# Optimization experiments

Hardware: AMD Instinct MI355X
Metric: run time of the kernel (lower is better)

Reference implementation:

```python
import jax, jax.numpy as jnp
import numpy as np

N_NODES = 100000
NEG_SLOPE = 0.2  # DGL GATConv default negative_slope


def gat_layer(x, src, dst, W, attn_l, attn_r, bias, n_nodes):
    """Single-head DGL GATConv. x: [N, in], returns [N, out]."""
    h = x @ W                              # [N, out]  fc (no bias)
    el = h @ attn_l                        # [N]
    er = h @ attn_r                        # [N]
    e = el[src] + er[dst]                  # [E]
    e = jnp.where(e >= 0, e, NEG_SLOPE * e)  # leaky_relu
    # segment softmax over incoming edges of each dst node
    m = jax.ops.segment_max(e, dst, num_segments=n_nodes)   # [N]
    ex = jnp.exp(e - m[dst])                                 # [E]
    s = jax.ops.segment_sum(ex, dst, num_segments=n_nodes)  # [N]
    a = ex / s[dst]                                          # [E]
    # weighted aggregate of source features
    msg = a[:, None] * h[src]                                # [E, out]
    out = jax.ops.segment_sum(msg, dst, num_segments=n_nodes)
    return out + bias


def setup_inputs() -> dict:
    key = jax.random.key(0)
    ks = jax.random.split(key, 12)
    n, e = N_NODES, 1600000
    in_f, hid_f, out_f = 128, 64, 64
    inp = {
        "features": jax.random.normal(ks[0], (n, in_f), dtype=jnp.float32),
        "edge_weights": jax.random.uniform(ks[1], (e,), dtype=jnp.float32),
        "src": jax.random.randint(ks[2], (e,), 0, n, dtype=jnp.int32),
        "dst": jax.random.randint(ks[3], (e,), 0, n, dtype=jnp.int32),
        "W1": jax.random.normal(ks[4], (in_f, hid_f), dtype=jnp.float32) * (1.0 / np.sqrt(in_f)),
        "attn_l1": jax.random.normal(ks[5], (hid_f,), dtype=jnp.float32) * 0.1,
        "attn_r1": jax.random.normal(ks[6], (hid_f,), dtype=jnp.float32) * 0.1,
        "bias1": jnp.zeros((hid_f,), dtype=jnp.float32),
        "W2": jax.random.normal(ks[7], (hid_f, out_f), dtype=jnp.float32) * (1.0 / np.sqrt(hid_f)),
        "attn_l2": jax.random.normal(ks[8], (out_f,), dtype=jnp.float32) * 0.1,
        "attn_r2": jax.random.normal(ks[9], (out_f,), dtype=jnp.float32) * 0.1,
        "bias2": jnp.zeros((out_f,), dtype=jnp.float32),
    }
    return inp


def reference(features, edge_weights, src, dst, W1, attn_l1, attn_r1, bias1,
              W2, attn_l2, attn_r2, bias2):
    n = features.shape[0]
    # conv1 -> DGL returns [N, 1, hid]; relu; conv2 -> [N, 1, 1, out]
    h = gat_layer(features, src, dst, W1, attn_l1, attn_r1, bias1, n)  # [N, hid]
    h = jax.nn.relu(h)
    out = gat_layer(h, src, dst, W2, attn_l2, attn_r2, bias2, n)       # [N, out]
    # edge_weights is accepted but unused, matching the original forward
    return out.reshape(n, 1, 1, -1)
```

## Files before the change

### kernel.cpp

```cpp
#include <hip/hip_runtime.h>
#include <hip/hip_fp16.h>

#define NEG_SLOPE 0.2f
#define BKT_SHIFT 9
#define BKT_SIZE (1 << BKT_SHIFT)
#define P1_EPT 16

typedef __attribute__((ext_vector_type(8))) short short8;
typedef __attribute__((ext_vector_type(4))) float float4v;

__device__ inline float readlane_f(float v, int l) {
    return __int_as_float(__builtin_amdgcn_readlane(__float_as_int(v), l));
}
__device__ inline int readlane_i(int v, int l) {
    return __builtin_amdgcn_readlane(v, l);
}
__device__ inline int rfl_i(int v) { return __builtin_amdgcn_readfirstlane(v); }

__device__ inline unsigned short f2bf(float f) {
    unsigned u = __float_as_uint(f);
    unsigned r = u + 0x7FFFu + ((u >> 16) & 1u);
    return (unsigned short)(r >> 16);
}
__device__ inline float bf2f(unsigned short b) {
    return __uint_as_float(((unsigned)b) << 16);
}


__global__ __launch_bounds__(256) void bucket_hist(const int* __restrict__ dst, int e,
                                                   int* __restrict__ bkt_cnt, int nbkt) {
    __shared__ int lc[256];
    int t = threadIdx.x;
    lc[t] = 0;
    __syncthreads();
    int stride = gridDim.x * blockDim.x;
    for (int i = blockIdx.x * blockDim.x + t; i < e; i += stride)
        atomicAdd(&lc[dst[i] >> BKT_SHIFT], 1);
    __syncthreads();
    if (t < nbkt && lc[t]) atomicAdd(&bkt_cnt[t], lc[t]);
}

__global__ void bkt_scan(const int* __restrict__ bkt_cnt, int* __restrict__ bbase,
                         int* __restrict__ gcur, int nbkt, int e_total) {
    __shared__ int tmp[256];
    int t = threadIdx.x;
    int v = (t < nbkt) ? bkt_cnt[t] : 0;
    tmp[t] = v;
    __syncthreads();
    for (int o = 1; o < 256; o <<= 1) {
        int x = tmp[t];
        int y = (t >= o) ? tmp[t - o] : 0;
        __syncthreads();
        tmp[t] = x + y;
        __syncthreads();
    }
    if (t < nbkt) {
        int ex = tmp[t] - v;
        bbase[t] = ex;
        gcur[t] = ex;
    }
    if (t == 0) bbase[nbkt] = e_total;
}

__global__ __launch_bounds__(256) void partition_kernel(
        const int* __restrict__ src, const int* __restrict__ dst, int e,
        int* __restrict__ gcur, int2* __restrict__ part, int nbkt) {
    __shared__ int cnt[4][256];
    __shared__ int base_l[4][256];
    int t = threadIdx.x;
    int wv = t >> 6;
    int cb = blockIdx.x * (256 * P1_EPT);
    for (int i = t; i < 4 * 256; i += 256) ((int*)cnt)[i] = 0;
    __syncthreads();
    int sr[P1_EPT], ds[P1_EPT], rk[P1_EPT];
#pragma unroll
    for (int i = 0; i < P1_EPT; ++i) {
        int eid = cb + t + i * 256;
        if (eid < e) {
            sr[i] = src[eid];
            ds[i] = dst[eid];
            rk[i] = atomicAdd(&cnt[wv][ds[i] >> BKT_SHIFT], 1);
        } else {
            rk[i] = -1;
        }
    }
    __syncthreads();
    if (t < nbkt) {
        int c0 = cnt[0][t], c1 = cnt[1][t], c2 = cnt[2][t], c3 = cnt[3][t];
        int tot = c0 + c1 + c2 + c3;
        int gb = (tot > 0) ? atomicAdd(&gcur[t], tot) : 0;
        base_l[0][t] = gb;
        base_l[1][t] = gb + c0;
        base_l[2][t] = gb + c0 + c1;
        base_l[3][t] = gb + c0 + c1 + c2;
    }
    __syncthreads();
#pragma unroll
    for (int i = 0; i < P1_EPT; ++i) {
        if (rk[i] >= 0) {
            int b = ds[i] >> BKT_SHIFT;
            part[base_l[wv][b] + rk[i]] = make_int2(sr[i], ds[i]);
        }
    }
}

__global__ __launch_bounds__(256) void finesort2(
        const int2* __restrict__ part, const int* __restrict__ bbase,
        int* __restrict__ row_off, int* __restrict__ csr_src, int n, int e_total) {
    __shared__ int cnt[BKT_SIZE];
    __shared__ int cur[BKT_SIZE];
    __shared__ int tmp[256];
    int b = blockIdx.x, t = threadIdx.x;
    int d0 = b << BKT_SHIFT;
    int dlim = min(d0 + BKT_SIZE, n);
    int nloc = dlim - d0;
    for (int i = t; i < BKT_SIZE; i += 256) cnt[i] = 0;
    __syncthreads();
    int base = bbase[b], bend = bbase[b + 1];
    for (int i = base + t; i < bend; i += 256)
        atomicAdd(&cnt[part[i].y - d0], 1);
    __syncthreads();
    int c0 = cnt[2 * t], c1 = cnt[2 * t + 1];
    int s = c0 + c1;
    tmp[t] = s;
    __syncthreads();
    for (int o = 1; o < 256; o <<= 1) {
        int x = tmp[t];
        int y = (t >= o) ? tmp[t - o] : 0;
        __syncthreads();
        tmp[t] = x + y;
        __syncthreads();
    }
    int excl = tmp[t] - s;
    cur[2 * t] = base + excl;
    cur[2 * t + 1] = base + excl + c0;
    __syncthreads();
    for (int i = t; i < nloc; i += 256) row_off[d0 + i] = cur[i];
    if (dlim == n && t == 0) row_off[n] = e_total;
    __syncthreads();
    for (int i = base + t; i < bend; i += 256) {
        int2 p = part[i];
        int pos = atomicAdd(&cur[p.y - d0], 1);
        csr_src[pos] = p.x;
    }
}

__global__ void wprep_kernel(const float* __restrict__ W, unsigned short* __restrict__ wh,
                             unsigned short* __restrict__ wl, int K) {
    int idx = blockIdx.x * blockDim.x + threadIdx.x;
    int KT = K / 32;
    if (idx >= KT * 4 * 64) return;
    int lane = idx & 63;
    int fbkt = idx >> 6;
    int fb = fbkt & 3, kt = fbkt >> 2;
    int q = lane >> 4, c = lane & 15;
    for (int j = 0; j < 8; ++j) {
        float w = W[(kt * 32 + q * 8 + j) * 64 + fb * 16 + c];
        unsigned short hi = f2bf(w);
        wh[idx * 8 + j] = hi;
        wl[idx * 8 + j] = f2bf(w - bf2f(hi));
    }
}

template <int KT>
__global__ __launch_bounds__(256) void gemm_mfma_kernel(
        const float* __restrict__ x, const unsigned short* __restrict__ wh,
        const unsigned short* __restrict__ wl,
        const float* __restrict__ al, const float* __restrict__ ar,
        __half* __restrict__ h16, float* __restrict__ el,
        float* __restrict__ er, int n) {
    constexpr int K = KT * 32;
    constexpr int WFRAG = KT * 4 * 64 * 8;
    __shared__ unsigned short Wh[WFRAG];
    __shared__ unsigned short Wl[WFRAG];
    for (int i = threadIdx.x; i < WFRAG / 8; i += 256) {
        ((float4*)Wh)[i] = ((const float4*)wh)[i];
        ((float4*)Wl)[i] = ((const float4*)wl)[i];
    }
    __syncthreads();

    int lane = threadIdx.x & 63;
    int q = lane >> 4, c = lane & 15;
    int wave = (int)((blockIdx.x * blockDim.x + threadIdx.x) >> 6);
    int nwaves = (gridDim.x * blockDim.x) >> 6;
    int ntiles = (n + 15) >> 4;

    float alv[4], arv[4];
#pragma unroll
    for (int fb = 0; fb < 4; ++fb) {
        alv[fb] = al[fb * 16 + c];
        arv[fb] = ar[fb * 16 + c];
    }

    for (int t = wave; t < ntiles; t += nwaves) {
        int v0 = t * 16;
        int row = min(v0 + c, n - 1);
        const float* xr = x + (size_t)row * K + q * 8;

        short8 Ah[KT], Al[KT];
#pragma unroll
        for (int kt = 0; kt < KT; ++kt) {
            float xv[8];
            *(float4*)&xv[0] = *(const float4*)(xr + kt * 32);
            *(float4*)&xv[4] = *(const float4*)(xr + kt * 32 + 4);
#pragma unroll
            for (int j = 0; j < 8; ++j) {
                unsigned short hi = f2bf(xv[j]);
                Ah[kt][j] = (short)hi;
                Al[kt][j] = (short)f2bf(xv[j] - bf2f(hi));
            }
        }

        float4v acc[4];
#pragma unroll
        for (int fb = 0; fb < 4; ++fb) acc[fb] = (float4v)0.f;

#pragma unroll
        for (int kt = 0; kt < KT; ++kt) {
#pragma unroll
            for (int fb = 0; fb < 4; ++fb) {
                short8 bh = *(const short8*)&Wh[((kt * 4 + fb) * 64 + lane) * 8];
                short8 bl = *(const short8*)&Wl[((kt * 4 + fb) * 64 + lane) * 8];
                acc[fb] = __builtin_amdgcn_mfma_f32_16x16x32_bf16(Ah[kt], bh, acc[fb], 0, 0, 0);
                acc[fb] = __builtin_amdgcn_mfma_f32_16x16x32_bf16(Al[kt], bh, acc[fb], 0, 0, 0);
                acc[fb] = __builtin_amdgcn_mfma_f32_16x16x32_bf16(Ah[kt], bl, acc[fb], 0, 0, 0);
            }
        }

#pragma unroll
        for (int r = 0; r < 4; ++r) {
            int v = v0 + q * 4 + r;
            float pl = 0.f, pr = 0.f;
            bool ok = (v < n);
#pragma unroll
            for (int fb = 0; fb < 4; ++fb) {
                float hv = acc[fb][r];
                if (ok) h16[(size_t)v * 64 + fb * 16 + c] = __float2half(hv);
                pl = fmaf(hv, alv[fb], pl);
                pr = fmaf(hv, arv[fb], pr);
            }
#pragma unroll
            for (int off = 8; off > 0; off >>= 1) {
                pl += __shfl_xor(pl, off);
                pr += __shfl_xor(pr, off);
            }
            if (ok && c == 0) { el[v] = pl; er[v] = pr; }
        }
    }
}

__global__ __launch_bounds__(256) void agg_kernel(
        const int* __restrict__ row_off, const int* __restrict__ csr_src,
        const __half* __restrict__ h16, const float* __restrict__ el,
        const float* __restrict__ er, const float* __restrict__ bias,
        float* __restrict__ out, int n, int do_relu) {
    int lane = threadIdx.x & 63;
    int gwave = rfl_i((int)((blockIdx.x * blockDim.x + threadIdx.x) >> 6));
    int nwaves = (gridDim.x * blockDim.x) >> 6;
    float b = bias[lane];
    for (int v = gwave; v < n; v += nwaves) {
        int rs = rfl_i(row_off[v]), re = rfl_i(row_off[v + 1]);
        float er_v = er[v];
        float acc = 0.f, ssum = 0.f;
        for (int base = rs; base < re; base += 64) {
            int cnt = min(64, re - base);
            int s_e = 0;
            float ex = 0.f;
            if (lane < cnt) {
                s_e = csr_src[base + lane];
                float ev = el[s_e] + er_v;
                ev = (ev >= 0.f) ? ev : NEG_SLOPE * ev;
                ex = __expf(ev);
            }
            float cs = ex;
#pragma unroll
            for (int off = 32; off > 0; off >>= 1) cs += __shfl_xor(cs, off);
            ssum += cs;
            int cnt8 = (cnt + 7) & ~7;
            for (int j = 0; j < cnt8; j += 8) {
                int sj[8];
                float exj[8];
                __half hv[8];
#pragma unroll
                for (int u = 0; u < 8; ++u) {
                    sj[u] = readlane_i(s_e, j + u);
                    exj[u] = readlane_f(ex, j + u);
                    hv[u] = h16[(size_t)sj[u] * 64 + lane];
                }
#pragma unroll
                for (int u = 0; u < 8; ++u)
                    acc = fmaf(exj[u], __half2float(hv[u]), acc);
            }
        }
        float o = (re > rs) ? (acc / ssum + b) : b;
        if (do_relu) o = fmaxf(o, 0.f);
        out[(size_t)v * 64 + lane] = o;
    }
}

extern "C" void kernel_launch(void* const* d_in, const int* in_sizes, int n_in,
                              void* d_out, int out_size, void* d_ws, size_t ws_size,
                              hipStream_t stream) {
    (void)n_in; (void)out_size; (void)ws_size;
    const float* features = (const float*)d_in[0];
    const int*   src = (const int*)d_in[2];
    const int*   dst = (const int*)d_in[3];
    const float* W1  = (const float*)d_in[4];
    const float* al1 = (const float*)d_in[5];
    const float* ar1 = (const float*)d_in[6];
    const float* b1  = (const float*)d_in[7];
    const float* W2  = (const float*)d_in[8];
    const float* al2 = (const float*)d_in[9];
    const float* ar2 = (const float*)d_in[10];
    const float* b2  = (const float*)d_in[11];

    const int n = in_sizes[0] / 128;
    const int e = in_sizes[2];
    float* out = (float*)d_out;

    char* p = (char*)d_ws;
    auto alloc = [&](size_t bytes) -> char* {
        char* q = p;
        p += (bytes + 255) & ~(size_t)255;
        return q;
    };
    int*    row_off = (int*)alloc((size_t)(n + 1) * 4);
    int*    csr_src = (int*)alloc((size_t)e * 4);
    __half* h16     = (__half*)alloc((size_t)n * 64 * 2);
    float*  hr      = (float*)alloc((size_t)n * 64 * 4);
    float*  el      = (float*)alloc((size_t)n * 4);
    float*  er      = (float*)alloc((size_t)n * 4);
    int*    bkt_cnt = (int*)alloc(256 * 4);
    int*    bbase   = (int*)alloc(257 * 4);
    int*    gcur    = (int*)alloc(256 * 4);
    unsigned short* w1h = (unsigned short*)alloc(4 * 4 * 64 * 8 * 2);
    unsigned short* w1l = (unsigned short*)alloc(4 * 4 * 64 * 8 * 2);
    unsigned short* w2h = (unsigned short*)alloc(2 * 4 * 64 * 8 * 2);
    unsigned short* w2l = (unsigned short*)alloc(2 * 4 * 64 * 8 * 2);
    int2*   part    = (int2*)hr;

    const int nbkt = (n + BKT_SIZE - 1) >> BKT_SHIFT;

    wprep_kernel<<<4, 256, 0, stream>>>(W1, w1h, w1l, 128);
    wprep_kernel<<<2, 256, 0, stream>>>(W2, w2h, w2l, 64);

    hipMemsetAsync(bkt_cnt, 0, 256 * 4, stream);
    bucket_hist<<<1024, 256, 0, stream>>>(dst, e, bkt_cnt, nbkt);
    bkt_scan<<<1, 256, 0, stream>>>(bkt_cnt, bbase, gcur, nbkt, e);
    partition_kernel<<<(e + 256 * P1_EPT - 1) / (256 * P1_EPT), 256, 0, stream>>>(
        src, dst, e, gcur, part, nbkt);
    finesort2<<<nbkt, 256, 0, stream>>>(part, bbase, row_off, csr_src, n, e);

    gemm_mfma_kernel<4><<<512, 256, 0, stream>>>(features, w1h, w1l, al1, ar1, h16, el, er, n);
    agg_kernel<<<2048, 256, 0, stream>>>(row_off, csr_src, h16, el, er, b1, hr, n, 1);

    gemm_mfma_kernel<2><<<512, 256, 0, stream>>>(hr, w2h, w2l, al2, ar2, h16, el, er, n);
    agg_kernel<<<2048, 256, 0, stream>>>(row_off, csr_src, h16, el, er, b2, out, n, 0);
}
```

Measured before the change: 299.5 us.

## Pack partition entries into one int and vectorize aggregation gathers per lane-group

```diff
diff --git a/kernel.cpp b/kernel.cpp
--- a/kernel.cpp
+++ b/kernel.cpp
@@ -11,9 +11,6 @@
 
 __device__ inline float readlane_f(float v, int l) {
     return __int_as_float(__builtin_amdgcn_readlane(__float_as_int(v), l));
-}
-__device__ inline int readlane_i(int v, int l) {
-    return __builtin_amdgcn_readlane(v, l);
 }
 __device__ inline int rfl_i(int v) { return __builtin_amdgcn_readfirstlane(v); }
 
@@ -64,7 +61,7 @@
 
 __global__ __launch_bounds__(256) void partition_kernel(
         const int* __restrict__ src, const int* __restrict__ dst, int e,
-        int* __restrict__ gcur, int2* __restrict__ part, int nbkt) {
+        int* __restrict__ gcur, int* __restrict__ part, int nbkt) {
     __shared__ int cnt[4][256];
     __shared__ int base_l[4][256];
     int t = threadIdx.x;
@@ -99,13 +96,13 @@
     for (int i = 0; i < P1_EPT; ++i) {
         if (rk[i] >= 0) {
             int b = ds[i] >> BKT_SHIFT;
-            part[base_l[wv][b] + rk[i]] = make_int2(sr[i], ds[i]);
+            part[base_l[wv][b] + rk[i]] = (sr[i] << BKT_SHIFT) | (ds[i] & (BKT_SIZE - 1));
         }
     }
 }
 
 __global__ __launch_bounds__(256) void finesort2(
-        const int2* __restrict__ part, const int* __restrict__ bbase,
+        const int* __restrict__ part, const int* __restrict__ bbase,
         int* __restrict__ row_off, int* __restrict__ csr_src, int n, int e_total) {
     __shared__ int cnt[BKT_SIZE];
     __shared__ int cur[BKT_SIZE];
@@ -118,7 +115,7 @@
     __syncthreads();
     int base = bbase[b], bend = bbase[b + 1];
     for (int i = base + t; i < bend; i += 256)
-        atomicAdd(&cnt[part[i].y - d0], 1);
+        atomicAdd(&cnt[part[i] & (BKT_SIZE - 1)], 1);
     __syncthreads();
     int c0 = cnt[2 * t], c1 = cnt[2 * t + 1];
     int s = c0 + c1;
@@ -139,9 +136,9 @@
     if (dlim == n && t == 0) row_off[n] = e_total;
     __syncthreads();
     for (int i = base + t; i < bend; i += 256) {
-        int2 p = part[i];
-        int pos = atomicAdd(&cur[p.y - d0], 1);
-        csr_src[pos] = p.x;
+        int pk = part[i];
+        int pos = atomicAdd(&cur[pk & (BKT_SIZE - 1)], 1);
+        csr_src[pos] = ((unsigned)pk) >> BKT_SHIFT;
     }
 }
 
@@ -255,13 +252,15 @@
         const float* __restrict__ er, const float* __restrict__ bias,
         float* __restrict__ out, int n, int do_relu) {
     int lane = threadIdx.x & 63;
+    int grp = lane >> 4;
+    int c = lane & 15;
     int gwave = rfl_i((int)((blockIdx.x * blockDim.x + threadIdx.x) >> 6));
     int nwaves = (gridDim.x * blockDim.x) >> 6;
-    float b = bias[lane];
+    float4 b4 = ((const float4*)bias)[c];
     for (int v = gwave; v < n; v += nwaves) {
         int rs = rfl_i(row_off[v]), re = rfl_i(row_off[v + 1]);
         float er_v = er[v];
-        float acc = 0.f, ssum = 0.f;
+        float a0 = 0.f, a1 = 0.f, a2 = 0.f, a3 = 0.f, ssum = 0.f;
         for (int base = rs; base < re; base += 64) {
             int cnt = min(64, re - base);
             int s_e = 0;
@@ -276,25 +275,55 @@
 #pragma unroll
             for (int off = 32; off > 0; off >>= 1) cs += __shfl_xor(cs, off);
             ssum += cs;
-            int cnt8 = (cnt + 7) & ~7;
-            for (int j = 0; j < cnt8; j += 8) {
-                int sj[8];
-                float exj[8];
-                __half hv[8];
-#pragma unroll
-                for (int u = 0; u < 8; ++u) {
-                    sj[u] = readlane_i(s_e, j + u);
-                    exj[u] = readlane_f(ex, j + u);
-                    hv[u] = h16[(size_t)sj[u] * 64 + lane];
+            int cnt16 = (cnt + 15) & ~15;
+            for (int j = 0; j < cnt16; j += 16) {
+                int sj[4];
+                float exj[4];
+                uint2 hv[4];
+#pragma unroll
+                for (int u = 0; u < 4; ++u) {
+                    int idx = j + 4 * u + grp;
+                    sj[u] = __shfl(s_e, idx);
+                    exj[u] = __shfl(ex, idx);
+                    hv[u] = *((const uint2*)(h16 + (size_t)sj[u] * 64) + c);
                 }
 #pragma unroll
-                for (int u = 0; u < 8; ++u)
-                    acc = fmaf(exj[u], __half2float(hv[u]), acc);
-            }
-        }
-        float o = (re > rs) ? (acc / ssum + b) : b;
-        if (do_relu) o = fmaxf(o, 0.f);
-        out[(size_t)v * 64 + lane] = o;
+                for (int u = 0; u < 4; ++u) {
+                    float2 f01 = __half22float2(*(__half2*)&hv[u].x);
+                    float2 f23 = __half22float2(*(__half2*)&hv[u].y);
+                    a0 = fmaf(exj[u], f01.x, a0);
+                    a1 = fmaf(exj[u], f01.y, a1);
+                    a2 = fmaf(exj[u], f23.x, a2);
+                    a3 = fmaf(exj[u], f23.y, a3);
+                }
+            }
+        }
+#pragma unroll
+        for (int off = 16; off < 64; off <<= 1) {
+            a0 += __shfl_xor(a0, off);
+            a1 += __shfl_xor(a1, off);
+            a2 += __shfl_xor(a2, off);
+            a3 += __shfl_xor(a3, off);
+        }
+        if (lane < 16) {
+            float4 o;
+            if (re > rs) {
+                float inv = 1.0f / ssum;
+                o.x = fmaf(a0, inv, b4.x);
+                o.y = fmaf(a1, inv, b4.y);
+                o.z = fmaf(a2, inv, b4.z);
+                o.w = fmaf(a3, inv, b4.w);
+            } else {
+                o = b4;
+            }
+            if (do_relu) {
+                o.x = fmaxf(o.x, 0.f);
+                o.y = fmaxf(o.y, 0.f);
+                o.z = fmaxf(o.z, 0.f);
+                o.w = fmaxf(o.w, 0.f);
+            }
+            ((float4*)(out + (size_t)v * 64))[c] = o;
+        }
     }
 }
 
@@ -337,7 +366,7 @@
     unsigned short* w1l = (unsigned short*)alloc(4 * 4 * 64 * 8 * 2);
     unsigned short* w2h = (unsigned short*)alloc(2 * 4 * 64 * 8 * 2);
     unsigned short* w2l = (unsigned short*)alloc(2 * 4 * 64 * 8 * 2);
-    int2*   part    = (int2*)hr;
+    int*    part    = (int*)hr;
 
     const int nbkt = (n + BKT_SIZE - 1) >> BKT_SHIFT;
 
```

Result: faster. 281.5 us (-6.0%).
